# Performance work log

Hardware: AMD Instinct MI355X
Metric: run time of the kernel (lower is better)

## Reference

```python
import jax, jax.numpy as jnp
import numpy as np

N, T, D_MODEL, H, DK = 4, 4096, 1024, 16, 64


def setup_inputs() -> dict:
    key = jax.random.key(0)
    ks = jax.random.split(key, 16)
    randn = lambda k, sh: jax.random.normal(k, sh, dtype=jnp.float32)
    # linear weights stored (in, out) so y = x @ W + b (math-equivalent to torch Linear)
    scale = 1.0 / np.sqrt(D_MODEL)
    return {
        "x_k": randn(ks[0], (N, T, D_MODEL)),
        "x_v": randn(ks[1], (N, T, D_MODEL)),
        "x_q": randn(ks[2], (N, T, D_MODEL)),
        "mask": jnp.ones((N, T), dtype=jnp.int32),
        "Wk": randn(ks[3], (D_MODEL, H * DK)) * scale,
        "bk": randn(ks[4], (H * DK,)) * 0.02,
        "Wv": randn(ks[5], (D_MODEL, H * DK)) * scale,
        "bv": randn(ks[6], (H * DK,)) * 0.02,
        "Wq": randn(ks[7], (D_MODEL, H * DK)) * scale,
        "bq": randn(ks[8], (H * DK,)) * 0.02,
        "alpha_w": randn(ks[9], (DK,)),
        "beta_w": randn(ks[10], (DK,)),
        "Wr": randn(ks[11], (DK, DK)) * (1.0 / np.sqrt(DK)),
        "br": randn(ks[12], (DK,)) * 0.02,
        "Wfc": randn(ks[13], (H * DK, D_MODEL)) * scale,
        "bfc": randn(ks[14], (D_MODEL,)) * 0.02,
    }


def _split_heads(x):  # (n, t, h*d) -> (n, h, t, d)
    n, t, _ = x.shape
    return x.reshape(n, t, H, DK).transpose(0, 2, 1, 3)


def reference(x_k, x_v, x_q, mask, Wk, bk, Wv, bv, Wq, bq,
              alpha_w, beta_w, Wr, br, Wfc, bfc):
    scale = DK ** (-0.5)
    k = _split_heads(x_k @ Wk + bk)  # (n, h, t, d)
    v = _split_heads(x_v @ Wv + bv)
    q = _split_heads(x_q @ Wq + bq)

    m = (mask == 0)[:, None, :]  # (n, 1, t) True where masked
    neg_inf = jnp.finfo(q.dtype).min

    # alpha pooling over queries -> global query (n, h, d)
    alpha = jnp.einsum('nhtd,d->nht', q, alpha_w) * scale
    alpha = jnp.where(m, neg_inf, alpha)
    alpha = jax.nn.softmax(alpha, axis=-1)
    global_query = jnp.einsum('nht,nhtd->nhd', alpha, q)

    # p = broadcast(global_query) * k, then beta pooling -> global key
    p = global_query[:, :, None, :] * k  # (n, h, t, d)
    beta = jnp.einsum('nhtd,d->nht', p, beta_w) * scale
    beta = jnp.where(m, neg_inf, beta)
    beta = jax.nn.softmax(beta, axis=-1)
    global_key = jnp.einsum('nht,nhtd->nhd', beta, p)

    u = global_key[:, :, None, :] * v  # (n, h, t, d)
    u_r = u @ Wr + br
    A = u_r + q  # (n, h, t, d)
    A = A.transpose(0, 2, 1, 3).reshape(N, T, H * DK)
    return A @ Wfc + bfc
```

## Files before the change

kernel.cpp:

```cpp
#include <hip/hip_runtime.h>

typedef __bf16 bf16x8 __attribute__((ext_vector_type(8)));
typedef float f32x4 __attribute__((ext_vector_type(4)));
typedef unsigned int u32x4 __attribute__((ext_vector_type(4)));
typedef unsigned short u16x4 __attribute__((ext_vector_type(4)));
typedef unsigned short u16x8 __attribute__((ext_vector_type(8)));

#define SEQ_T 4096
#define DMODEL 1024
#define HEADS 16
#define DKH 64
#define MTOK 16384

#define AS1 __attribute__((address_space(1)))
#define AS3 __attribute__((address_space(3)))

__device__ __forceinline__ unsigned short f2bf(float f) {
  unsigned u = __builtin_bit_cast(unsigned int, f);
  u += 0x7FFFu + ((u >> 16) & 1u);
  return (unsigned short)(u >> 16);
}
__device__ __forceinline__ float bf2f(unsigned short h) {
  unsigned u = ((unsigned)h) << 16;
  return __builtin_bit_cast(float, u);
}
__device__ __forceinline__ void gload16(const unsigned short* g, unsigned short* l) {
  __builtin_amdgcn_global_load_lds((const AS1 unsigned int*)(g),
                                   (AS3 unsigned int*)(l), 16, 0, 0);
}

__global__ void __launch_bounds__(256) k_cvt(const float* __restrict__ x,
                                             unsigned short* __restrict__ y,
                                             long long nelem) {
  long long i = ((long long)blockIdx.x * 256 + threadIdx.x) * 8;
  if (i >= nelem) return;
  u16x8 o;
#pragma unroll
  for (int j = 0; j < 8; ++j) o[j] = f2bf(x[i + j]);
  *(u16x8*)(y + i) = o;
}

__global__ void __launch_bounds__(256) k_wtrans(const float* __restrict__ W,
                                                unsigned short* __restrict__ Wt,
                                                int K, int N) {
  __shared__ float tile[32][33];
  int bn = blockIdx.x * 32, bk = blockIdx.y * 32;
  int tx = threadIdx.x, ty = threadIdx.y;
#pragma unroll
  for (int j = 0; j < 32; j += 8)
    tile[ty + j][tx] = W[(size_t)(bk + ty + j) * N + bn + tx];
  __syncthreads();
#pragma unroll
  for (int j = 0; j < 32; j += 8)
    Wt[(size_t)(bn + ty + j) * K + bk + tx] = f2bf(tile[tx][ty + j]);
}

#define BM 128
#define BN 128
#define BK 32

template <int OBF, int SCORE, int FUSEA>
__global__ void __launch_bounds__(256, 2)
k_gemm(const unsigned short* __restrict__ A, const unsigned short* __restrict__ Bt,
       const float* __restrict__ bias, void* __restrict__ C,
       const int* __restrict__ mask, const float* __restrict__ swt,
       float* __restrict__ sbuf, const unsigned short* __restrict__ qadd,
       int M, int N, int K) {
  __shared__ unsigned short As[BM * BK];
  __shared__ unsigned short Bs[BN * BK];
  const int tid = threadIdx.x;
  const int lane = tid & 63, wid = tid >> 6;
  const int wr = wid >> 1, wc = wid & 1;
  const int bnb = blockIdx.x;
  const int bm = blockIdx.y * BM, bn = bnb * BN;
  const int l15 = lane & 15, l4 = lane >> 4;

  const unsigned short* Btn = FUSEA ? Bt + ((size_t)(bm >> 12) << 20) : Bt;
  const float* biasn = FUSEA ? bias + ((bm >> 12) << 10) : bias;

  f32x4 acc[4][4];
#pragma unroll
  for (int i = 0; i < 4; ++i)
#pragma unroll
    for (int j = 0; j < 4; ++j)
#pragma unroll
      for (int e = 0; e < 4; ++e) acc[i][j][e] = 0.f;

  const int srow = wid * 32 + (lane >> 2);
  const int scol = (lane & 3) * 8;
  const unsigned short* Ag = A + (size_t)(bm + srow) * K + scol;
  const unsigned short* Bg = Btn + (size_t)(bn + srow) * K + scol;
  unsigned short* Al = As + wid * 32 * BK;
  unsigned short* Bl = Bs + wid * 32 * BK;

  for (int kt = 0; kt < K; kt += BK) {
    __syncthreads();
    gload16(Ag + kt, Al);
    gload16(Ag + kt + 16 * K, Al + 16 * BK);
    gload16(Bg + kt, Bl);
    gload16(Bg + kt + 16 * K, Bl + 16 * BK);
    __syncthreads();
    bf16x8 af[4], bfr[4];
#pragma unroll
    for (int m = 0; m < 4; ++m)
      af[m] = *(const bf16x8*)(As + (wr * 64 + m * 16 + l15) * BK + l4 * 8);
#pragma unroll
    for (int n = 0; n < 4; ++n)
      bfr[n] = *(const bf16x8*)(Bs + (wc * 64 + n * 16 + l15) * BK + l4 * 8);
#pragma unroll
    for (int m = 0; m < 4; ++m)
#pragma unroll
      for (int n = 0; n < 4; ++n)
        acc[m][n] = __builtin_amdgcn_mfma_f32_16x16x32_bf16(af[m], bfr[n],
                                                            acc[m][n], 0, 0, 0);
  }

  const int crow = bm + wr * 64 + l4 * 4;
  const int ccol = bn + wc * 64 + l15;

  float pacc[4][4];
  const float* wrow = nullptr;
  if (SCORE == 1) wrow = swt;
  if (SCORE) {
#pragma unroll
    for (int m = 0; m < 4; ++m)
#pragma unroll
      for (int e = 0; e < 4; ++e) pacc[m][e] = 0.f;
  }

#pragma unroll
  for (int m = 0; m < 4; ++m)
#pragma unroll
    for (int n = 0; n < 4; ++n) {
      int c = ccol + n * 16;
      float bj = biasn[c];
      float wg = SCORE ? wrow[n * 16 + l15] : 0.f;
#pragma unroll
      for (int e = 0; e < 4; ++e) {
        int r = crow + m * 16 + e;
        float v = acc[m][n][e] + bj;
        if (FUSEA) v += bf2f(qadd[(size_t)r * N + c]);
        if (SCORE) pacc[m][e] += v * wg;
        if (OBF)
          ((unsigned short*)C)[(size_t)r * N + c] = f2bf(v);
        else
          ((float*)C)[(size_t)r * N + c] = v;
      }
    }

  if (SCORE) {
#pragma unroll
    for (int m = 0; m < 4; ++m)
#pragma unroll
      for (int e = 0; e < 4; ++e) {
        float p = pacc[m][e];
        p += __shfl_xor(p, 1);
        p += __shfl_xor(p, 2);
        p += __shfl_xor(p, 4);
        p += __shfl_xor(p, 8);
        if (l15 == 0) {
          int r = crow + m * 16 + e;
          int t = r & (SEQ_T - 1), n = r >> 12;
          float sc = p * 0.125f;
          if (mask[n * SEQ_T + t] == 0) sc = -3.0e38f;
          sbuf[((size_t)n * HEADS + bnb * 2 + wc) * SEQ_T + t] = sc;
        }
      }
  }
}

__global__ void __launch_bounds__(256) k_stat1(const float* __restrict__ s,
                                               float* __restrict__ pmax,
                                               float* __restrict__ psum) {
  __shared__ float red[4];
  const int b = blockIdx.x, tid = threadIdx.x, lane = tid & 63, wid = tid >> 6;
  float v = s[(size_t)b * 256 + tid];
  float m = v;
#pragma unroll
  for (int o = 1; o < 64; o <<= 1) m = fmaxf(m, __shfl_xor(m, o));
  if (lane == 0) red[wid] = m;
  __syncthreads();
  m = fmaxf(fmaxf(red[0], red[1]), fmaxf(red[2], red[3]));
  __syncthreads();
  float e = __expf(v - m);
#pragma unroll
  for (int o = 1; o < 64; o <<= 1) e += __shfl_xor(e, o);
  if (lane == 0) red[wid] = e;
  __syncthreads();
  if (tid == 0) {
    pmax[b] = m;
    psum[b] = red[0] + red[1] + red[2] + red[3];
  }
}

__global__ void __launch_bounds__(64) k_stat2(const float* __restrict__ pmax,
                                              const float* __restrict__ psum,
                                              float* __restrict__ smx,
                                              float* __restrict__ sinv) {
  const int b = blockIdx.x, lane = threadIdx.x;
  float pm = -3.4e38f, ps = 0.f;
  if (lane < 16) {
    pm = pmax[b * 16 + lane];
    ps = psum[b * 16 + lane];
  }
  float gm = pm;
#pragma unroll
  for (int o = 1; o < 16; o <<= 1) gm = fmaxf(gm, __shfl_xor(gm, o));
  float sc = ps * __expf(pm - gm);
#pragma unroll
  for (int o = 1; o < 16; o <<= 1) sc += __shfl_xor(sc, o);
  if (lane == 0) {
    smx[b] = gm;
    sinv[b] = 1.f / sc;
  }
}

__global__ void __launch_bounds__(256) k_wsum(const unsigned short* __restrict__ X,
                                              const float* __restrict__ s,
                                              const float* __restrict__ mxv,
                                              const float* __restrict__ invv,
                                              float* __restrict__ pbuf) {
  __shared__ float part[16][64];
  const int nh = blockIdx.x >> 4, chunk = blockIdx.x & 15;
  const int n = nh >> 4, h = nh & 15;
  const int tid = threadIdx.x, lane = tid & 63, wid = tid >> 6;
  const int tsub = lane >> 4, dl = lane & 15;
  const float mx = mxv[nh], inv = invv[nh];
  const float* sb = s + (size_t)nh * SEQ_T + chunk * 256;
  const size_t base = ((size_t)n * SEQ_T + chunk * 256) * DMODEL + h * DKH + dl * 4;
  f32x4 acc = {0.f, 0.f, 0.f, 0.f};
  for (int t = wid * 4 + tsub; t < 256; t += 16) {
    float w = __expf(sb[t] - mx) * inv;
    u16x4 xv = *(const u16x4*)(X + base + (size_t)t * DMODEL);
    acc[0] += w * bf2f(xv[0]);
    acc[1] += w * bf2f(xv[1]);
    acc[2] += w * bf2f(xv[2]);
    acc[3] += w * bf2f(xv[3]);
  }
  int g = wid * 4 + tsub;
#pragma unroll
  for (int e = 0; e < 4; ++e) part[g][dl * 4 + e] = acc[e];
  __syncthreads();
  if (tid < 64) {
    float v = 0.f;
#pragma unroll
    for (int gg = 0; gg < 16; ++gg) v += part[gg][tid];
    pbuf[(size_t)blockIdx.x * 64 + tid] = v;
  }
}

__global__ void __launch_bounds__(64) k_fin(const float* __restrict__ pbuf,
                                            const float* __restrict__ bw,
                                            float* __restrict__ out,
                                            float* __restrict__ wv) {
  const int nh = blockIdx.x, d = threadIdx.x;
  float v = 0.f;
#pragma unroll
  for (int c = 0; c < 16; ++c) v += pbuf[((size_t)nh * 16 + c) * 64 + d];
  out[(size_t)nh * 64 + d] = v;
  wv[(size_t)nh * 64 + d] = v * bw[d];
}

__global__ void __launch_bounds__(256) k_wks(const float* __restrict__ Wk,
                                             const float* __restrict__ wv,
                                             unsigned short* __restrict__ WksT) {
  const int nh = blockIdx.x, tid = threadIdx.x;
  const int n = nh >> 4, h = nh & 15;
  __shared__ float wvs[64];
  if (tid < 64) wvs[tid] = wv[(size_t)nh * 64 + tid];
  __syncthreads();
  int c0 = tid * 4;
  u16x4 o;
#pragma unroll
  for (int i = 0; i < 4; ++i) {
    int c = c0 + i;
    const float* wr = Wk + (size_t)c * DMODEL + h * DKH;
    float acc = 0.f;
#pragma unroll
    for (int dd = 0; dd < 64; dd += 4) {
      f32x4 w4 = *(const f32x4*)(wr + dd);
      acc += w4[0] * wvs[dd] + w4[1] * wvs[dd + 1] + w4[2] * wvs[dd + 2] +
             w4[3] * wvs[dd + 3];
    }
    o[i] = f2bf(acc);
  }
  *(u16x4*)(WksT + (size_t)n * 16 * DMODEL + (size_t)h * DMODEL + c0) = o;
}

__global__ void __launch_bounds__(64) k_bks(const float* __restrict__ bk,
                                            const float* __restrict__ wv,
                                            float* __restrict__ bks) {
  const int nh = blockIdx.x, dd = threadIdx.x;
  const int h = nh & 15;
  float p = bk[h * 64 + dd] * wv[(size_t)nh * 64 + dd];
#pragma unroll
  for (int o = 1; o < 64; o <<= 1) p += __shfl_xor(p, o);
  if (dd == 0) bks[nh] = p;
}

__global__ void __launch_bounds__(128) k_score(const unsigned short* __restrict__ xk,
                                               const unsigned short* __restrict__ WksT,
                                               const float* __restrict__ bks,
                                               const int* __restrict__ mask,
                                               float* __restrict__ sbuf) {
  __shared__ unsigned short Xs[64 * 32];
  __shared__ unsigned short Ws[16 * 32];
  const int tid = threadIdx.x, lane = tid & 63, wid = tid >> 6;
  const int l15 = lane & 15, l4 = lane >> 4;
  const int bm = blockIdx.x * 64;
  const int n = bm >> 12;
  const unsigned short* Wn = WksT + (size_t)n * 16 * DMODEL;

  f32x4 acc[2];
#pragma unroll
  for (int m = 0; m < 2; ++m)
#pragma unroll
    for (int e = 0; e < 4; ++e) acc[m][e] = 0.f;

  const int srow = lane >> 2, scol = (lane & 3) * 8;
  for (int kt = 0; kt < DMODEL; kt += 32) {
    __syncthreads();
#pragma unroll
    for (int j = 0; j < 2; ++j) {
      int rb = wid * 32 + j * 16;
      gload16(xk + (size_t)(bm + rb + srow) * DMODEL + kt + scol, Xs + rb * 32);
    }
    if (wid == 0) gload16(Wn + (size_t)srow * DMODEL + kt + scol, Ws);
    __syncthreads();
    bf16x8 bfr = *(const bf16x8*)(Ws + l15 * 32 + l4 * 8);
#pragma unroll
    for (int m = 0; m < 2; ++m) {
      bf16x8 af = *(const bf16x8*)(Xs + (wid * 32 + m * 16 + l15) * 32 + l4 * 8);
      acc[m] = __builtin_amdgcn_mfma_f32_16x16x32_bf16(af, bfr, acc[m], 0, 0, 0);
    }
  }
  const int h = l15;
  const float bh = bks[n * 16 + h];
#pragma unroll
  for (int m = 0; m < 2; ++m)
#pragma unroll
    for (int e = 0; e < 4; ++e) {
      int r = bm + wid * 32 + m * 16 + l4 * 4 + e;
      int t = r & (SEQ_T - 1);
      float sc = (acc[m][e] + bh) * 0.125f;
      if (mask[n * SEQ_T + t] == 0) sc = -3.0e38f;
      sbuf[((size_t)n * HEADS + h) * SEQ_T + t] = sc;
    }
}

__global__ void __launch_bounds__(256) k_bwsum(const float* __restrict__ xk,
                                               const float* __restrict__ s,
                                               const float* __restrict__ smx,
                                               const float* __restrict__ sinv,
                                               float* __restrict__ part) {
  __shared__ float eb[16][64];
  const int tc = blockIdx.x, n = blockIdx.y, tid = threadIdx.x;
#pragma unroll
  for (int i = 0; i < 4; ++i) {
    int idx = i * 256 + tid;
    int h = idx >> 6, t = idx & 63;
    int nh = n * 16 + h;
    eb[h][t] = __expf(s[(size_t)nh * SEQ_T + tc * 64 + t] - smx[nh]) * sinv[nh];
  }
  __syncthreads();
  const int c0 = tid * 4;
  f32x4 acc[16];
#pragma unroll
  for (int h = 0; h < 16; ++h)
#pragma unroll
    for (int e = 0; e < 4; ++e) acc[h][e] = 0.f;
  const float* xb = xk + ((size_t)n * SEQ_T + tc * 64) * DMODEL + c0;
  for (int t = 0; t < 64; ++t) {
    f32x4 x = *(const f32x4*)(xb + (size_t)t * DMODEL);
#pragma unroll
    for (int h = 0; h < 16; ++h) {
      float w = eb[h][t];
      acc[h][0] += w * x[0];
      acc[h][1] += w * x[1];
      acc[h][2] += w * x[2];
      acc[h][3] += w * x[3];
    }
  }
#pragma unroll
  for (int h = 0; h < 16; ++h)
    *(f32x4*)(part + (((size_t)(n * 64 + tc)) * 16 + h) * DMODEL + c0) = acc[h];
}

__global__ void __launch_bounds__(256) k_bred(const float* __restrict__ part,
                                              float* __restrict__ pooled) {
  const int nh = blockIdx.x, tid = threadIdx.x;
  const int n = nh >> 4, h = nh & 15;
  const int c0 = tid * 4;
  f32x4 acc = {0.f, 0.f, 0.f, 0.f};
  for (int tc = 0; tc < 64; ++tc) {
    f32x4 p = *(const f32x4*)(part + (((size_t)(n * 64 + tc)) * 16 + h) * DMODEL + c0);
    acc[0] += p[0]; acc[1] += p[1]; acc[2] += p[2]; acc[3] += p[3];
  }
  *(f32x4*)(pooled + (size_t)nh * DMODEL + c0) = acc;
}

__global__ void __launch_bounds__(64) k_gk(const float* __restrict__ pooled,
                                           const unsigned short* __restrict__ WkT,
                                           const float* __restrict__ bk,
                                           const float* __restrict__ gq,
                                           float* __restrict__ gk) {
  __shared__ float pl[DMODEL];
  const int nh = blockIdx.x, dd = threadIdx.x;
  const int h = nh & 15;
#pragma unroll
  for (int i = 0; i < 16; ++i) pl[i * 64 + dd] = pooled[(size_t)nh * DMODEL + i * 64 + dd];
  __syncthreads();
  const unsigned short* wr = WkT + (size_t)(h * 64 + dd) * DMODEL;
  float acc = 0.f;
  for (int c = 0; c < DMODEL; c += 8) {
    u16x8 w = *(const u16x8*)(wr + c);
#pragma unroll
    for (int j = 0; j < 8; ++j) acc += pl[c + j] * bf2f(w[j]);
  }
  gk[(size_t)nh * 64 + dd] = gq[(size_t)nh * 64 + dd] * (acc + bk[h * 64 + dd]);
}

__global__ void __launch_bounds__(256) k_wrg(const float* __restrict__ gk,
                                             const float* __restrict__ Wr,
                                             unsigned short* __restrict__ WrgT) {
  const int nh = blockIdx.x, tid = threadIdx.x;
#pragma unroll
  for (int i = 0; i < 16; ++i) {
    int idx = i * 256 + tid;
    int d = idx >> 6, dd = idx & 63;
    WrgT[(size_t)nh * 4096 + idx] = f2bf(gk[nh * 64 + dd] * Wr[dd * 64 + d]);
  }
}

#define LDW 72
__global__ void __launch_bounds__(256) k_wcomb(const unsigned short* __restrict__ WrgT,
                                               const unsigned short* __restrict__ WvN,
                                               unsigned short* __restrict__ WcombT) {
  __shared__ unsigned short Wg[64 * LDW];
  __shared__ unsigned short Vv[128 * LDW];
  const int rc = blockIdx.x, nh = blockIdx.y;
  const int n = nh >> 4, h = nh & 15;
  const int tid = threadIdx.x, lane = tid & 63, wid = tid >> 6;
  const int l15 = lane & 15, l4 = lane >> 4;
#pragma unroll
  for (int i = 0; i < 2; ++i) {
    int v = i * 256 + tid;
    int d = v >> 3, k8 = v & 7;
    *(u16x8*)(Wg + d * LDW + k8 * 8) =
        *(const u16x8*)(WrgT + (size_t)nh * 4096 + d * 64 + k8 * 8);
  }
#pragma unroll
  for (int i = 0; i < 4; ++i) {
    int v = i * 256 + tid;
    int r = v >> 3, k8 = v & 7;
    *(u16x8*)(Vv + r * LDW + k8 * 8) =
        *(const u16x8*)(WvN + (size_t)(rc * 128 + r) * DMODEL + h * 64 + k8 * 8);
  }
  __syncthreads();
  f32x4 acc[8];
#pragma unroll
  for (int ct = 0; ct < 8; ++ct)
#pragma unroll
    for (int e = 0; e < 4; ++e) acc[ct][e] = 0.f;
#pragma unroll
  for (int ks = 0; ks < 2; ++ks) {
    bf16x8 af = *(const bf16x8*)(Wg + (wid * 16 + l15) * LDW + ks * 32 + l4 * 8);
#pragma unroll
    for (int ct = 0; ct < 8; ++ct) {
      bf16x8 bf = *(const bf16x8*)(Vv + (ct * 16 + l15) * LDW + ks * 32 + l4 * 8);
      acc[ct] = __builtin_amdgcn_mfma_f32_16x16x32_bf16(af, bf, acc[ct], 0, 0, 0);
    }
  }
  unsigned short* out = WcombT + ((size_t)n << 20);
#pragma unroll
  for (int ct = 0; ct < 8; ++ct)
#pragma unroll
    for (int e = 0; e < 4; ++e) {
      int d = h * 64 + wid * 16 + l4 * 4 + e;
      int r = rc * 128 + ct * 16 + l15;
      out[(size_t)d * DMODEL + r] = f2bf(acc[ct][e]);
    }
}

__global__ void __launch_bounds__(64) k_bcomb(const float* __restrict__ bv,
                                              const unsigned short* __restrict__ WrgT,
                                              const float* __restrict__ br,
                                              float* __restrict__ bcomb) {
  const int nh = blockIdx.x, d = threadIdx.x;
  const int n = nh >> 4, h = nh & 15;
  float acc = br[d];
#pragma unroll
  for (int dd = 0; dd < 64; ++dd)
    acc += bv[h * 64 + dd] * bf2f(WrgT[(size_t)nh * 4096 + d * 64 + dd]);
  bcomb[(size_t)n * DMODEL + h * 64 + d] = acc;
}

extern "C" void kernel_launch(void* const* d_in, const int* in_sizes, int n_in,
                              void* d_out, int out_size, void* d_ws, size_t ws_size,
                              hipStream_t stream) {
  const float* x_k = (const float*)d_in[0];
  const float* x_v = (const float*)d_in[1];
  const float* x_q = (const float*)d_in[2];
  const int* mask = (const int*)d_in[3];
  const float* Wk = (const float*)d_in[4];
  const float* bk = (const float*)d_in[5];
  const float* Wv = (const float*)d_in[6];
  const float* bv = (const float*)d_in[7];
  const float* Wq = (const float*)d_in[8];
  const float* bq = (const float*)d_in[9];
  const float* alpha_w = (const float*)d_in[10];
  const float* beta_w = (const float*)d_in[11];
  const float* Wr = (const float*)d_in[12];
  const float* br = (const float*)d_in[13];
  const float* Wfc = (const float*)d_in[14];
  const float* bfc = (const float*)d_in[15];

  unsigned short* qbf = (unsigned short*)d_out;

  char* ws = (char*)d_ws;
  const size_t MB = 1024 * 1024;
  unsigned short* xst = (unsigned short*)(ws);
  unsigned short* abuf = (unsigned short*)(ws + 32 * MB);
  unsigned short* WqT = (unsigned short*)(ws + 64 * MB);
  unsigned short* WkT = WqT + (size_t)DMODEL * DMODEL;
  unsigned short* WfT = WkT + (size_t)DMODEL * DMODEL;
  unsigned short* WvN = WfT + (size_t)DMODEL * DMODEL;
  unsigned short* WcombT = WvN + (size_t)DMODEL * DMODEL;
  unsigned short* WrgT = WcombT + (size_t)4 * DMODEL * DMODEL;
  unsigned short* WksT = WrgT + (size_t)64 * 4096;
  float* part = (float*)(WksT + (size_t)4 * 16 * DMODEL);
  float* pooled = part + (size_t)256 * 16 * DMODEL;
  float* sbuf = pooled + (size_t)64 * DMODEL;
  float* pbuf = sbuf + (size_t)64 * SEQ_T;
  float* pmax = pbuf + 1024 * 64;
  float* psum = pmax + 1024;
  float* smx = psum + 1024;
  float* sinv = smx + 64;
  float* gq = sinv + 64;
  float* wvb = gq + 4096;
  float* gk = wvb + 4096;
  float* bks = gk + 4096;
  float* bcomb = bks + 64;

  dim3 tb(32, 8);
  dim3 tg(DMODEL / 32, DMODEL / 32);
  k_wtrans<<<tg, tb, 0, stream>>>(Wq, WqT, DMODEL, DMODEL);
  k_wtrans<<<tg, tb, 0, stream>>>(Wk, WkT, DMODEL, DMODEL);
  k_wtrans<<<tg, tb, 0, stream>>>(Wfc, WfT, DMODEL, DMODEL);
  k_cvt<<<512, 256, 0, stream>>>(Wv, WvN, (long long)DMODEL * DMODEL);

  long long nx = (long long)MTOK * DMODEL;
  int cvtg = (int)(nx / 8 / 256);
  dim3 ggrid(DMODEL / BN, MTOK / BM);

  k_cvt<<<cvtg, 256, 0, stream>>>(x_q, xst, nx);
  k_gemm<1, 1, 0><<<ggrid, 256, 0, stream>>>(xst, WqT, bq, (void*)qbf, mask,
                                             alpha_w, sbuf, nullptr,
                                             MTOK, DMODEL, DMODEL);
  k_stat1<<<1024, 256, 0, stream>>>(sbuf, pmax, psum);
  k_stat2<<<64, 64, 0, stream>>>(pmax, psum, smx, sinv);
  k_wsum<<<1024, 256, 0, stream>>>(qbf, sbuf, smx, sinv, pbuf);
  k_fin<<<64, 64, 0, stream>>>(pbuf, beta_w, gq, wvb);

  k_wks<<<64, 256, 0, stream>>>(Wk, wvb, WksT);
  k_bks<<<64, 64, 0, stream>>>(bk, wvb, bks);
  k_cvt<<<cvtg, 256, 0, stream>>>(x_k, xst, nx);
  k_score<<<MTOK / 64, 128, 0, stream>>>(xst, WksT, bks, mask, sbuf);
  k_stat1<<<1024, 256, 0, stream>>>(sbuf, pmax, psum);
  k_stat2<<<64, 64, 0, stream>>>(pmax, psum, smx, sinv);
  dim3 bwg(64, 4);
  k_bwsum<<<bwg, 256, 0, stream>>>(x_k, sbuf, smx, sinv, part);
  k_bred<<<64, 256, 0, stream>>>(part, pooled);
  k_gk<<<64, 64, 0, stream>>>(pooled, WkT, bk, gq, gk);

  k_wrg<<<64, 256, 0, stream>>>(gk, Wr, WrgT);
  dim3 wcg(8, 64);
  k_wcomb<<<wcg, 256, 0, stream>>>(WrgT, WvN, WcombT);
  k_bcomb<<<64, 64, 0, stream>>>(bv, WrgT, br, bcomb);

  k_cvt<<<cvtg, 256, 0, stream>>>(x_v, xst, nx);
  k_gemm<1, 0, 1><<<ggrid, 256, 0, stream>>>(xst, WcombT, bcomb, (void*)abuf,
                                             nullptr, nullptr, nullptr, qbf,
                                             MTOK, DMODEL, DMODEL);

  k_gemm<0, 0, 0><<<ggrid, 256, 0, stream>>>(abuf, WfT, bfc, d_out, nullptr,
                                             nullptr, nullptr, nullptr,
                                             MTOK, DMODEL, DMODEL);
}
```

Measured before the change: 320.5 us.

## Widen GEMM K-tile with XOR-swizzled LDS and fuse small reduction kernels

The GEMM K-tile grows from 32 to 64 and shared-memory rows use an XOR swizzle to avoid bank conflicts, which halves the number of barrier pairs per K loop. Several tiny kernels are merged: the two-stage softmax stats become one kernel per head, k_wks absorbs k_bks, k_bred absorbs k_gk, and k_wrg absorbs k_bcomb. k_bwsum now reads the bf16-converted x_k instead of the fp32 input, halving that read traffic. The trade-offs are fewer blocks for the softmax stats (64 instead of 1024), more LDS per GEMM block, and the bcomb bias now computed from unrounded fp32 values rather than bf16.

```diff
diff --git a/kernel.cpp b/kernel.cpp
--- a/kernel.cpp
+++ b/kernel.cpp
@@ -57,7 +57,7 @@
 
 #define BM 128
 #define BN 128
-#define BK 32
+#define BK 64
 
 template <int OBF, int SCORE, int FUSEA>
 __global__ void __launch_bounds__(256, 2)
@@ -86,33 +86,44 @@
 #pragma unroll
       for (int e = 0; e < 4; ++e) acc[i][j][e] = 0.f;
 
-  const int srow = wid * 32 + (lane >> 2);
-  const int scol = (lane & 3) * 8;
-  const unsigned short* Ag = A + (size_t)(bm + srow) * K + scol;
-  const unsigned short* Bg = Btn + (size_t)(bn + srow) * K + scol;
-  unsigned short* Al = As + wid * 32 * BK;
-  unsigned short* Bl = Bs + wid * 32 * BK;
+  const int sgr = lane >> 3;
+  const int sgc = (lane & 7) ^ sgr;
 
   for (int kt = 0; kt < K; kt += BK) {
     __syncthreads();
-    gload16(Ag + kt, Al);
-    gload16(Ag + kt + 16 * K, Al + 16 * BK);
-    gload16(Bg + kt, Bl);
-    gload16(Bg + kt + 16 * K, Bl + 16 * BK);
+#pragma unroll
+    for (int j = 0; j < 4; ++j) {
+      int rb = wid * 32 + j * 8;
+      gload16(A + (size_t)(bm + rb + sgr) * K + kt + sgc * 8, As + rb * BK);
+    }
+#pragma unroll
+    for (int j = 0; j < 4; ++j) {
+      int rb = wid * 32 + j * 8;
+      gload16(Btn + (size_t)(bn + rb + sgr) * K + kt + sgc * 8, Bs + rb * BK);
+    }
     __syncthreads();
-    bf16x8 af[4], bfr[4];
-#pragma unroll
-    for (int m = 0; m < 4; ++m)
-      af[m] = *(const bf16x8*)(As + (wr * 64 + m * 16 + l15) * BK + l4 * 8);
-#pragma unroll
-    for (int n = 0; n < 4; ++n)
-      bfr[n] = *(const bf16x8*)(Bs + (wc * 64 + n * 16 + l15) * BK + l4 * 8);
-#pragma unroll
-    for (int m = 0; m < 4; ++m)
-#pragma unroll
-      for (int n = 0; n < 4; ++n)
-        acc[m][n] = __builtin_amdgcn_mfma_f32_16x16x32_bf16(af[m], bfr[n],
-                                                            acc[m][n], 0, 0, 0);
+#pragma unroll
+    for (int kh = 0; kh < 2; ++kh) {
+      bf16x8 af[4], bfr[4];
+#pragma unroll
+      for (int m = 0; m < 4; ++m) {
+        int ra = wr * 64 + m * 16 + l15;
+        int sl = (kh * 4 + l4) ^ (ra & 7);
+        af[m] = *(const bf16x8*)(As + ra * BK + sl * 8);
+      }
+#pragma unroll
+      for (int n = 0; n < 4; ++n) {
+        int rb = wc * 64 + n * 16 + l15;
+        int sl = (kh * 4 + l4) ^ (rb & 7);
+        bfr[n] = *(const bf16x8*)(Bs + rb * BK + sl * 8);
+      }
+#pragma unroll
+      for (int m = 0; m < 4; ++m)
+#pragma unroll
+        for (int n = 0; n < 4; ++n)
+          acc[m][n] = __builtin_amdgcn_mfma_f32_16x16x32_bf16(af[m], bfr[n],
+                                                              acc[m][n], 0, 0, 0);
+    }
   }
 
   const int crow = bm + wr * 64 + l4 * 4;
@@ -169,49 +180,29 @@
   }
 }
 
-__global__ void __launch_bounds__(256) k_stat1(const float* __restrict__ s,
-                                               float* __restrict__ pmax,
-                                               float* __restrict__ psum) {
+__global__ void __launch_bounds__(256) k_softmax(const float* __restrict__ s,
+                                                 float* __restrict__ mxo,
+                                                 float* __restrict__ invo) {
   __shared__ float red[4];
-  const int b = blockIdx.x, tid = threadIdx.x, lane = tid & 63, wid = tid >> 6;
-  float v = s[(size_t)b * 256 + tid];
-  float m = v;
+  const int tid = threadIdx.x, lane = tid & 63, wid = tid >> 6;
+  const float* sb = s + (size_t)blockIdx.x * SEQ_T;
+  float m = -3.4e38f;
+  for (int t = tid; t < SEQ_T; t += 256) m = fmaxf(m, sb[t]);
 #pragma unroll
   for (int o = 1; o < 64; o <<= 1) m = fmaxf(m, __shfl_xor(m, o));
   if (lane == 0) red[wid] = m;
   __syncthreads();
   m = fmaxf(fmaxf(red[0], red[1]), fmaxf(red[2], red[3]));
   __syncthreads();
-  float e = __expf(v - m);
-#pragma unroll
-  for (int o = 1; o < 64; o <<= 1) e += __shfl_xor(e, o);
-  if (lane == 0) red[wid] = e;
+  float sum = 0.f;
+  for (int t = tid; t < SEQ_T; t += 256) sum += __expf(sb[t] - m);
+#pragma unroll
+  for (int o = 1; o < 64; o <<= 1) sum += __shfl_xor(sum, o);
+  if (lane == 0) red[wid] = sum;
   __syncthreads();
   if (tid == 0) {
-    pmax[b] = m;
-    psum[b] = red[0] + red[1] + red[2] + red[3];
-  }
-}
-
-__global__ void __launch_bounds__(64) k_stat2(const float* __restrict__ pmax,
-                                              const float* __restrict__ psum,
-                                              float* __restrict__ smx,
-                                              float* __restrict__ sinv) {
-  const int b = blockIdx.x, lane = threadIdx.x;
-  float pm = -3.4e38f, ps = 0.f;
-  if (lane < 16) {
-    pm = pmax[b * 16 + lane];
-    ps = psum[b * 16 + lane];
-  }
-  float gm = pm;
-#pragma unroll
-  for (int o = 1; o < 16; o <<= 1) gm = fmaxf(gm, __shfl_xor(gm, o));
-  float sc = ps * __expf(pm - gm);
-#pragma unroll
-  for (int o = 1; o < 16; o <<= 1) sc += __shfl_xor(sc, o);
-  if (lane == 0) {
-    smx[b] = gm;
-    sinv[b] = 1.f / sc;
+    mxo[blockIdx.x] = m;
+    invo[blockIdx.x] = 1.f / (red[0] + red[1] + red[2] + red[3]);
   }
 }
 
@@ -261,9 +252,11 @@
   wv[(size_t)nh * 64 + d] = v * bw[d];
 }
 
-__global__ void __launch_bounds__(256) k_wks(const float* __restrict__ Wk,
-                                             const float* __restrict__ wv,
-                                             unsigned short* __restrict__ WksT) {
+__global__ void __launch_bounds__(256) k_wksb(const float* __restrict__ Wk,
+                                              const float* __restrict__ bk,
+                                              const float* __restrict__ wv,
+                                              unsigned short* __restrict__ WksT,
+                                              float* __restrict__ bks) {
   const int nh = blockIdx.x, tid = threadIdx.x;
   const int n = nh >> 4, h = nh & 15;
   __shared__ float wvs[64];
@@ -285,17 +278,12 @@
     o[i] = f2bf(acc);
   }
   *(u16x4*)(WksT + (size_t)n * 16 * DMODEL + (size_t)h * DMODEL + c0) = o;
-}
-
-__global__ void __launch_bounds__(64) k_bks(const float* __restrict__ bk,
-                                            const float* __restrict__ wv,
-                                            float* __restrict__ bks) {
-  const int nh = blockIdx.x, dd = threadIdx.x;
-  const int h = nh & 15;
-  float p = bk[h * 64 + dd] * wv[(size_t)nh * 64 + dd];
-#pragma unroll
-  for (int o = 1; o < 64; o <<= 1) p += __shfl_xor(p, o);
-  if (dd == 0) bks[nh] = p;
+  if (tid < 64) {
+    float p = bk[h * 64 + tid] * wvs[tid];
+#pragma unroll
+    for (int ofs = 1; ofs < 64; ofs <<= 1) p += __shfl_xor(p, ofs);
+    if (tid == 0) bks[nh] = p;
+  }
 }
 
 __global__ void __launch_bounds__(128) k_score(const unsigned short* __restrict__ xk,
@@ -348,7 +336,7 @@
     }
 }
 
-__global__ void __launch_bounds__(256) k_bwsum(const float* __restrict__ xk,
+__global__ void __launch_bounds__(256) k_bwsum(const unsigned short* __restrict__ xk,
                                                const float* __restrict__ s,
                                                const float* __restrict__ smx,
                                                const float* __restrict__ sinv,
@@ -369,16 +357,17 @@
   for (int h = 0; h < 16; ++h)
 #pragma unroll
     for (int e = 0; e < 4; ++e) acc[h][e] = 0.f;
-  const float* xb = xk + ((size_t)n * SEQ_T + tc * 64) * DMODEL + c0;
+  const unsigned short* xb = xk + ((size_t)n * SEQ_T + tc * 64) * DMODEL + c0;
   for (int t = 0; t < 64; ++t) {
-    f32x4 x = *(const f32x4*)(xb + (size_t)t * DMODEL);
+    u16x4 xr = *(const u16x4*)(xb + (size_t)t * DMODEL);
+    float x0 = bf2f(xr[0]), x1 = bf2f(xr[1]), x2 = bf2f(xr[2]), x3 = bf2f(xr[3]);
 #pragma unroll
     for (int h = 0; h < 16; ++h) {
       float w = eb[h][t];
-      acc[h][0] += w * x[0];
-      acc[h][1] += w * x[1];
-      acc[h][2] += w * x[2];
-      acc[h][3] += w * x[3];
+      acc[h][0] += w * x0;
+      acc[h][1] += w * x1;
+      acc[h][2] += w * x2;
+      acc[h][3] += w * x3;
     }
   }
 #pragma unroll
@@ -386,49 +375,58 @@
     *(f32x4*)(part + (((size_t)(n * 64 + tc)) * 16 + h) * DMODEL + c0) = acc[h];
 }
 
-__global__ void __launch_bounds__(256) k_bred(const float* __restrict__ part,
-                                              float* __restrict__ pooled) {
+__global__ void __launch_bounds__(256) k_gkr(const float* __restrict__ part,
+                                             const unsigned short* __restrict__ WkT,
+                                             const float* __restrict__ bk,
+                                             const float* __restrict__ gq,
+                                             float* __restrict__ gk) {
+  __shared__ float pl[DMODEL];
   const int nh = blockIdx.x, tid = threadIdx.x;
   const int n = nh >> 4, h = nh & 15;
   const int c0 = tid * 4;
-  f32x4 acc = {0.f, 0.f, 0.f, 0.f};
+  f32x4 a4 = {0.f, 0.f, 0.f, 0.f};
   for (int tc = 0; tc < 64; ++tc) {
     f32x4 p = *(const f32x4*)(part + (((size_t)(n * 64 + tc)) * 16 + h) * DMODEL + c0);
-    acc[0] += p[0]; acc[1] += p[1]; acc[2] += p[2]; acc[3] += p[3];
-  }
-  *(f32x4*)(pooled + (size_t)nh * DMODEL + c0) = acc;
-}
-
-__global__ void __launch_bounds__(64) k_gk(const float* __restrict__ pooled,
-                                           const unsigned short* __restrict__ WkT,
-                                           const float* __restrict__ bk,
-                                           const float* __restrict__ gq,
-                                           float* __restrict__ gk) {
-  __shared__ float pl[DMODEL];
-  const int nh = blockIdx.x, dd = threadIdx.x;
-  const int h = nh & 15;
-#pragma unroll
-  for (int i = 0; i < 16; ++i) pl[i * 64 + dd] = pooled[(size_t)nh * DMODEL + i * 64 + dd];
-  __syncthreads();
-  const unsigned short* wr = WkT + (size_t)(h * 64 + dd) * DMODEL;
-  float acc = 0.f;
-  for (int c = 0; c < DMODEL; c += 8) {
-    u16x8 w = *(const u16x8*)(wr + c);
-#pragma unroll
-    for (int j = 0; j < 8; ++j) acc += pl[c + j] * bf2f(w[j]);
-  }
-  gk[(size_t)nh * 64 + dd] = gq[(size_t)nh * 64 + dd] * (acc + bk[h * 64 + dd]);
-}
-
-__global__ void __launch_bounds__(256) k_wrg(const float* __restrict__ gk,
-                                             const float* __restrict__ Wr,
-                                             unsigned short* __restrict__ WrgT) {
+    a4[0] += p[0]; a4[1] += p[1]; a4[2] += p[2]; a4[3] += p[3];
+  }
+#pragma unroll
+  for (int e = 0; e < 4; ++e) pl[c0 + e] = a4[e];
+  __syncthreads();
+  if (tid < 64) {
+    const unsigned short* wr = WkT + (size_t)(h * 64 + tid) * DMODEL;
+    float acc = 0.f;
+    for (int c = 0; c < DMODEL; c += 8) {
+      u16x8 w = *(const u16x8*)(wr + c);
+#pragma unroll
+      for (int j = 0; j < 8; ++j) acc += pl[c + j] * bf2f(w[j]);
+    }
+    gk[(size_t)nh * 64 + tid] = gq[(size_t)nh * 64 + tid] * (acc + bk[h * 64 + tid]);
+  }
+}
+
+__global__ void __launch_bounds__(256) k_wrgb(const float* __restrict__ gk,
+                                              const float* __restrict__ Wr,
+                                              const float* __restrict__ bv,
+                                              const float* __restrict__ br,
+                                              unsigned short* __restrict__ WrgT,
+                                              float* __restrict__ bcomb) {
+  __shared__ float wl[4096];
   const int nh = blockIdx.x, tid = threadIdx.x;
+  const int n = nh >> 4, h = nh & 15;
 #pragma unroll
   for (int i = 0; i < 16; ++i) {
     int idx = i * 256 + tid;
     int d = idx >> 6, dd = idx & 63;
-    WrgT[(size_t)nh * 4096 + idx] = f2bf(gk[nh * 64 + dd] * Wr[dd * 64 + d]);
+    float v = gk[nh * 64 + dd] * Wr[dd * 64 + d];
+    wl[idx] = v;
+    WrgT[(size_t)nh * 4096 + idx] = f2bf(v);
+  }
+  __syncthreads();
+  if (tid < 64) {
+    float acc = br[tid];
+#pragma unroll
+    for (int dd = 0; dd < 64; ++dd) acc += bv[h * 64 + dd] * wl[tid * 64 + dd];
+    bcomb[(size_t)n * DMODEL + h * 64 + tid] = acc;
   }
 }
 
@@ -480,19 +478,6 @@
       int r = rc * 128 + ct * 16 + l15;
       out[(size_t)d * DMODEL + r] = f2bf(acc[ct][e]);
     }
-}
-
-__global__ void __launch_bounds__(64) k_bcomb(const float* __restrict__ bv,
-                                              const unsigned short* __restrict__ WrgT,
-                                              const float* __restrict__ br,
-                                              float* __restrict__ bcomb) {
-  const int nh = blockIdx.x, d = threadIdx.x;
-  const int n = nh >> 4, h = nh & 15;
-  float acc = br[d];
-#pragma unroll
-  for (int dd = 0; dd < 64; ++dd)
-    acc += bv[h * 64 + dd] * bf2f(WrgT[(size_t)nh * 4096 + d * 64 + dd]);
-  bcomb[(size_t)n * DMODEL + h * 64 + d] = acc;
 }
 
 extern "C" void kernel_launch(void* const* d_in, const int* in_sizes, int n_in,
@@ -532,9 +517,7 @@
   float* pooled = part + (size_t)256 * 16 * DMODEL;
   float* sbuf = pooled + (size_t)64 * DMODEL;
   float* pbuf = sbuf + (size_t)64 * SEQ_T;
-  float* pmax = pbuf + 1024 * 64;
-  float* psum = pmax + 1024;
-  float* smx = psum + 1024;
+  float* smx = pbuf + 1024 * 64;
   float* sinv = smx + 64;
   float* gq = sinv + 64;
   float* wvb = gq + 4096;
@@ -557,26 +540,21 @@
   k_gemm<1, 1, 0><<<ggrid, 256, 0, stream>>>(xst, WqT, bq, (void*)qbf, mask,
                                              alpha_w, sbuf, nullptr,
                                              MTOK, DMODEL, DMODEL);
-  k_stat1<<<1024, 256, 0, stream>>>(sbuf, pmax, psum);
-  k_stat2<<<64, 64, 0, stream>>>(pmax, psum, smx, sinv);
+  k_softmax<<<64, 256, 0, stream>>>(sbuf, smx, sinv);
   k_wsum<<<1024, 256, 0, stream>>>(qbf, sbuf, smx, sinv, pbuf);
   k_fin<<<64, 64, 0, stream>>>(pbuf, beta_w, gq, wvb);
 
-  k_wks<<<64, 256, 0, stream>>>(Wk, wvb, WksT);
-  k_bks<<<64, 64, 0, stream>>>(bk, wvb, bks);
+  k_wksb<<<64, 256, 0, stream>>>(Wk, bk, wvb, WksT, bks);
   k_cvt<<<cvtg, 256, 0, stream>>>(x_k, xst, nx);
   k_score<<<MTOK / 64, 128, 0, stream>>>(xst, WksT, bks, mask, sbuf);
-  k_stat1<<<1024, 256, 0, stream>>>(sbuf, pmax, psum);
-  k_stat2<<<64, 64, 0, stream>>>(pmax, psum, smx, sinv);
+  k_softmax<<<64, 256, 0, stream>>>(sbuf, smx, sinv);
   dim3 bwg(64, 4);
-  k_bwsum<<<bwg, 256, 0, stream>>>(x_k, sbuf, smx, sinv, part);
-  k_bred<<<64, 256, 0, stream>>>(part, pooled);
-  k_gk<<<64, 64, 0, stream>>>(pooled, WkT, bk, gq, gk);
-
-  k_wrg<<<64, 256, 0, stream>>>(gk, Wr, WrgT);
+  k_bwsum<<<bwg, 256, 0, stream>>>(xst, sbuf, smx, sinv, part);
+  k_gkr<<<64, 256, 0, stream>>>(part, WkT, bk, gq, gk);
+
+  k_wrgb<<<64, 256, 0, stream>>>(gk, Wr, bv, br, WrgT, bcomb);
   dim3 wcg(8, 64);
   k_wcomb<<<wcg, 256, 0, stream>>>(WrgT, WvN, WcombT);
-  k_bcomb<<<64, 64, 0, stream>>>(bv, WrgT, br, bcomb);
 
   k_cvt<<<cvtg, 256, 0, stream>>>(x_v, xst, nx);
   k_gemm<1, 0, 1><<<ggrid, 256, 0, stream>>>(xst, WcombT, bcomb, (void*)abuf,
```

Result: faster. 308.5 us (-3.8%).
